# Optimization experiments

Measured on AMD Instinct MI355X. Metric: run time of the kernel, lower is better.

Reference implementation:

```python
import jax, jax.numpy as jnp
import numpy as np

KP_VARIANCE = 0.01


def make_coordinate_grid(h, w, dtype):
    # Normalized coordinates in [-1, 1], last dim is (x, y) as in monkey-net.
    x = 2.0 * (jnp.arange(w, dtype=dtype) / (w - 1)) - 1.0
    y = 2.0 * (jnp.arange(h, dtype=dtype) / (h - 1)) - 1.0
    xx = jnp.broadcast_to(x[None, :], (h, w))
    yy = jnp.broadcast_to(y[:, None], (h, w))
    return jnp.stack([xx, yy], axis=-1)  # (h, w, 2)


def grid_sample_bilinear(img, grid):
    # img: (N, C, H, W), grid: (N, Hg, Wg, 2) with xy in [-1, 1].
    # Bilinear, align_corners=True, zero padding (torch grid_sample defaults in monkey-net era).
    N, C, H, W = img.shape
    x = (grid[..., 0] + 1.0) * (W - 1) * 0.5
    y = (grid[..., 1] + 1.0) * (H - 1) * 0.5
    x0 = jnp.floor(x); y0 = jnp.floor(y)
    x1 = x0 + 1.0;     y1 = y0 + 1.0
    wx1 = x - x0; wx0 = 1.0 - wx1
    wy1 = y - y0; wy0 = 1.0 - wy1

    def gather(ix, iy):
        valid = ((ix >= 0) & (ix <= W - 1) & (iy >= 0) & (iy <= H - 1)).astype(img.dtype)
        ixc = jnp.clip(ix, 0, W - 1).astype(jnp.int32)
        iyc = jnp.clip(iy, 0, H - 1).astype(jnp.int32)
        vals = jax.vmap(lambda im, yy_, xx_: im[:, yy_, xx_])(img, iyc, ixc)  # (N, C, Hg, Wg)
        return vals * valid[:, None, :, :]

    out = (gather(x0, y0) * (wx0 * wy0)[:, None]
           + gather(x1, y0) * (wx1 * wy0)[:, None]
           + gather(x0, y1) * (wx0 * wy1)[:, None]
           + gather(x1, y1) * (wx1 * wy1)[:, None])
    return out


def setup_inputs() -> dict:
    key = jax.random.key(0)
    k1, k2, k3 = jax.random.split(key, 3)
    bs, c, dsrc, h, w = 4, 3, 1, 128, 128
    d, K = 8, 10
    source_image = jax.random.uniform(k1, (bs, c, dsrc, h, w), jnp.float32)
    kp_driving_mean = jax.random.uniform(k2, (bs, d, K, 2), jnp.float32, minval=-1.0, maxval=1.0)
    kp_source_mean = jax.random.uniform(k3, (bs, d, K, 2), jnp.float32, minval=-1.0, maxval=1.0)
    return {"source_image": source_image,
            "kp_driving_mean": kp_driving_mean,
            "kp_source_mean": kp_source_mean}


def reference(source_image, kp_driving_mean, kp_source_mean):
    bs, c, dsrc, h, w = source_image.shape
    _, d, K, _ = kp_driving_mean.shape
    grid = make_coordinate_grid(h, w, source_image.dtype)  # (h, w, 2)

    # Gaussian heatmaps around driving keypoints: (bs, d, K, h, w)
    diff2 = ((grid - kp_driving_mean[:, :, :, None, None, :]) ** 2).sum(-1)
    heat = jnp.exp(-0.5 * diff2 / KP_VARIANCE)
    heat = heat / heat.sum(axis=(-2, -1), keepdims=True)  # norm_const == 'sum'
    # add background feature map (zeros) as kp index 0
    heat = jnp.concatenate([jnp.zeros((bs, d, 1, h, w), heat.dtype), heat], axis=2)
    K1 = K + 1

    # keypoint motion difference: (bs, d, K1, 2)
    kp_diff = kp_source_mean - kp_driving_mean
    kp_diff = jnp.concatenate([jnp.zeros((bs, d, 1, 2), kp_diff.dtype), kp_diff], axis=2)
    diff_map = jnp.broadcast_to(kp_diff[:, :, :, :, None, None], (bs, d, K1, 2, h, w))

    # deformed source image per (frame, keypoint)
    app = jnp.broadcast_to(source_image[:, None, None], (bs, d, K1, c, dsrc, h, w))
    app = app.reshape(bs * d * K1, c * dsrc, h, w)
    deform = grid[None] + kp_diff.reshape(bs * d * K1, 1, 1, 2)  # (N, h, w, 2)
    deformed = grid_sample_bilinear(app, deform).reshape(bs, d, K1, c * dsrc, h, w)

    enc = jnp.concatenate([heat[:, :, :, None], diff_map, deformed], axis=3)  # (bs,d,K1,1+2+c,h,w)
    enc = enc.reshape(bs, d, -1, h, w)
    enc = jnp.transpose(enc, (0, 2, 1, 3, 4))  # (bs, out_channels, d, h, w)
    return enc
```

## Files before the change

### kernel.cpp

```cpp
#include <hip/hip_runtime.h>
#include <math.h>

#define BS 4
#define C  3
#define D  8
#define K  10
#define K1 11
#define H  128
#define W  128
#define HW (H*W)

typedef float float4a __attribute__((ext_vector_type(4), aligned(4)));

__global__ void memb_norm_kernel(const float* __restrict__ kpd,
                                 float* __restrict__ norm) {
    int idx = blockIdx.x;
    float kx = kpd[idx * 2 + 0];
    float ky = kpd[idx * 2 + 1];
    int lane = threadIdx.x;
    float sx = 0.f, sy = 0.f;
    #pragma unroll
    for (int j = lane; j < W; j += 64) {
        float coord = (float)j * (2.0f / 127.0f) - 1.0f;
        float ddx = coord - kx;
        float ddy = coord - ky;
        sx += __expf(-50.0f * ddx * ddx);
        sy += __expf(-50.0f * ddy * ddy);
    }
    #pragma unroll
    for (int o = 32; o > 0; o >>= 1) {
        sx += __shfl_down(sx, o, 64);
        sy += __shfl_down(sy, o, 64);
    }
    if (lane == 0) norm[idx] = 1.0f / (sx * sy);
}

__global__ void memb_main_kernel(const float* __restrict__ src,
                                 const float* __restrict__ kpd,
                                 const float* __restrict__ kps,
                                 const float* __restrict__ norm,
                                 float* __restrict__ out) {
    int rk = blockIdx.y;
    int k  = rk % K1;
    int r  = rk / K1;
    int di = r & (D - 1);
    int b  = r >> 3;

    float kx = 0.f, ky = 0.f, dx = 0.f, dy = 0.f, nrm = 0.f;
    if (k > 0) {
        int kidx = r * K + (k - 1);
        kx  = kpd[kidx * 2 + 0];
        ky  = kpd[kidx * 2 + 1];
        dx  = kps[kidx * 2 + 0] - kx;
        dy  = kps[kidx * 2 + 1] - ky;
        nrm = norm[kidx];
    }

    int p   = (blockIdx.x * blockDim.x + threadIdx.x) << 2;
    int wi0 = p & (W - 1);
    int hi  = p >> 7;

    float y  = (float)hi * (2.0f / 127.0f) - 1.0f;
    float ey = y - ky;
    float expy = __expf(-50.0f * ey * ey) * nrm;
    float heat[4];
    #pragma unroll
    for (int j = 0; j < 4; j++) {
        float x  = (float)(wi0 + j) * (2.0f / 127.0f) - 1.0f;
        float ex = x - kx;
        heat[j] = expy * __expf(-50.0f * ex * ex);
    }

    float cx = 63.5f * dx, cy = 63.5f * dy;
    float fsx = floorf(cx), fsy = floorf(cy);
    float fx = cx - fsx,    fy = cy - fsy;
    int   sx = (int)fsx,    sy = (int)fsy;
    float wx0 = 1.0f - fx,  wx1 = fx;

    int iy0 = hi + sy, iy1 = iy0 + 1;
    float rv0 = (iy0 >= 0 && iy0 < H) ? (1.0f - fy) : 0.0f;
    float rv1 = (iy1 >= 0 && iy1 < H) ? fy : 0.0f;
    int cy0 = min(max(iy0, 0), H - 1);
    int cy1 = min(max(iy1, 0), H - 1);

    int c0 = wi0 + sx;
    const float* sb = src + (size_t)b * C * HW;

    float v[C][4];
    if (c0 >= 0 && c0 <= W - 5) {
        #pragma unroll
        for (int ci = 0; ci < C; ci++) {
            const float* r0 = sb + ci * HW + cy0 * W;
            const float* r1 = sb + ci * HW + cy1 * W;
            float4a a  = *(const float4a*)(r0 + c0);
            float   a4 = r0[c0 + 4];
            float4a bq = *(const float4a*)(r1 + c0);
            float   b4 = r1[c0 + 4];
            float m0 = rv0 * a[0] + rv1 * bq[0];
            float m1 = rv0 * a[1] + rv1 * bq[1];
            float m2 = rv0 * a[2] + rv1 * bq[2];
            float m3 = rv0 * a[3] + rv1 * bq[3];
            float m4 = rv0 * a4   + rv1 * b4;
            v[ci][0] = wx0 * m0 + wx1 * m1;
            v[ci][1] = wx0 * m1 + wx1 * m2;
            v[ci][2] = wx0 * m2 + wx1 * m3;
            v[ci][3] = wx0 * m3 + wx1 * m4;
        }
    } else {
        #pragma unroll
        for (int ci = 0; ci < C; ci++) {
            const float* r0 = sb + ci * HW + cy0 * W;
            const float* r1 = sb + ci * HW + cy1 * W;
            float m[5];
            #pragma unroll
            for (int i = 0; i < 5; i++) {
                int q = c0 + i;
                bool ok = (q >= 0) && (q < W);
                int qc = min(max(q, 0), W - 1);
                float mm = rv0 * r0[qc] + rv1 * r1[qc];
                m[i] = ok ? mm : 0.0f;
            }
            v[ci][0] = wx0 * m[0] + wx1 * m[1];
            v[ci][1] = wx0 * m[1] + wx1 * m[2];
            v[ci][2] = wx0 * m[2] + wx1 * m[3];
            v[ci][3] = wx0 * m[3] + wx1 * m[4];
        }
    }

    const size_t cs = (size_t)D * HW;
    size_t base = ((size_t)(b * 66 + k * 6) * D + di) * HW + (size_t)hi * W + wi0;
    *(float4*)(out + base + 0 * cs) = make_float4(heat[0], heat[1], heat[2], heat[3]);
    *(float4*)(out + base + 1 * cs) = make_float4(dx, dx, dx, dx);
    *(float4*)(out + base + 2 * cs) = make_float4(dy, dy, dy, dy);
    *(float4*)(out + base + 3 * cs) = make_float4(v[0][0], v[0][1], v[0][2], v[0][3]);
    *(float4*)(out + base + 4 * cs) = make_float4(v[1][0], v[1][1], v[1][2], v[1][3]);
    *(float4*)(out + base + 5 * cs) = make_float4(v[2][0], v[2][1], v[2][2], v[2][3]);
}

extern "C" void kernel_launch(void* const* d_in, const int* in_sizes, int n_in,
                              void* d_out, int out_size, void* d_ws, size_t ws_size,
                              hipStream_t stream) {
    const float* src = (const float*)d_in[0];
    const float* kpd = (const float*)d_in[1];
    const float* kps = (const float*)d_in[2];
    float* out  = (float*)d_out;
    float* norm = (float*)d_ws;

    memb_norm_kernel<<<BS * D * K, 64, 0, stream>>>(kpd, norm);

    dim3 grid(HW / (256 * 4), BS * D * K1);
    memb_main_kernel<<<grid, 256, 0, stream>>>(src, kpd, kps, norm, out);
}
```

Baseline: 149.8 us.

## Fuse norm computation into main kernel with shared-memory exp tables

Removes the separate normalization kernel: each block computes the per-keypoint x/y Gaussian tables in shared memory, reduces them to the normalization constant, and builds heatmaps from the separable tables. Each thread now produces 8 pixels instead of 4, with a tile of 16 rows per block and an early zero path for fully out-of-bounds samples. This saves one launch and most exp evaluations, at the cost of two block barriers and redundant table computation in every block.

```diff
diff --git a/kernel.cpp b/kernel.cpp
--- a/kernel.cpp
+++ b/kernel.cpp
@@ -12,129 +12,145 @@
 
 typedef float float4a __attribute__((ext_vector_type(4), aligned(4)));
 
-__global__ void memb_norm_kernel(const float* __restrict__ kpd,
-                                 float* __restrict__ norm) {
-    int idx = blockIdx.x;
-    float kx = kpd[idx * 2 + 0];
-    float ky = kpd[idx * 2 + 1];
-    int lane = threadIdx.x;
-    float sx = 0.f, sy = 0.f;
-    #pragma unroll
-    for (int j = lane; j < W; j += 64) {
-        float coord = (float)j * (2.0f / 127.0f) - 1.0f;
-        float ddx = coord - kx;
-        float ddy = coord - ky;
-        sx += __expf(-50.0f * ddx * ddx);
-        sy += __expf(-50.0f * ddy * ddy);
-    }
-    #pragma unroll
-    for (int o = 32; o > 0; o >>= 1) {
-        sx += __shfl_down(sx, o, 64);
-        sy += __shfl_down(sy, o, 64);
-    }
-    if (lane == 0) norm[idx] = 1.0f / (sx * sy);
-}
+__global__ __launch_bounds__(256) void memb_fused_kernel(
+        const float* __restrict__ src,
+        const float* __restrict__ kpd,
+        const float* __restrict__ kps,
+        float* __restrict__ out) {
+    __shared__ __align__(16) float s_expx[128];
+    __shared__ __align__(16) float s_expy[128];
+    __shared__ float s_red[4];
+    __shared__ float s_nrm;
 
-__global__ void memb_main_kernel(const float* __restrict__ src,
-                                 const float* __restrict__ kpd,
-                                 const float* __restrict__ kps,
-                                 const float* __restrict__ norm,
-                                 float* __restrict__ out) {
     int rk = blockIdx.y;
     int k  = rk % K1;
     int r  = rk / K1;
     int di = r & (D - 1);
     int b  = r >> 3;
 
-    float kx = 0.f, ky = 0.f, dx = 0.f, dy = 0.f, nrm = 0.f;
+    float kx = 0.f, ky = 0.f, dx = 0.f, dy = 0.f;
     if (k > 0) {
         int kidx = r * K + (k - 1);
-        kx  = kpd[kidx * 2 + 0];
-        ky  = kpd[kidx * 2 + 1];
-        dx  = kps[kidx * 2 + 0] - kx;
-        dy  = kps[kidx * 2 + 1] - ky;
-        nrm = norm[kidx];
+        kx = kpd[kidx * 2 + 0];
+        ky = kpd[kidx * 2 + 1];
+        dx = kps[kidx * 2 + 0] - kx;
+        dy = kps[kidx * 2 + 1] - ky;
     }
 
-    int p   = (blockIdx.x * blockDim.x + threadIdx.x) << 2;
-    int wi0 = p & (W - 1);
-    int hi  = p >> 7;
+    int tid = threadIdx.x;
 
-    float y  = (float)hi * (2.0f / 127.0f) - 1.0f;
-    float ey = y - ky;
-    float expy = __expf(-50.0f * ey * ey) * nrm;
-    float heat[4];
-    #pragma unroll
-    for (int j = 0; j < 4; j++) {
-        float x  = (float)(wi0 + j) * (2.0f / 127.0f) - 1.0f;
-        float ex = x - kx;
-        heat[j] = expy * __expf(-50.0f * ex * ex);
+    {
+        int j = tid & 127;
+        float coord = (float)j * (2.0f / 127.0f) - 1.0f;
+        float dd = coord - ((tid < 128) ? kx : ky);
+        float e = __expf(-50.0f * dd * dd);
+        if (tid < 128) s_expx[j] = e;
+        else           s_expy[j] = e;
+        #pragma unroll
+        for (int o = 32; o > 0; o >>= 1) e += __shfl_down(e, o, 64);
+        if ((tid & 63) == 0) s_red[tid >> 6] = e;
     }
+    __syncthreads();
+    if (tid == 0) {
+        float sumx = s_red[0] + s_red[1];
+        float sumy = s_red[2] + s_red[3];
+        s_nrm = (k > 0) ? (1.0f / (sumx * sumy)) : 0.0f;
+    }
+    __syncthreads();
+
+    int g   = tid >> 4;
+    int rr  = tid & 15;
+    int wi0 = g << 3;
+    int hi  = (blockIdx.x << 4) + rr;
+
+    float hy = s_expy[hi] * s_nrm;
 
     float cx = 63.5f * dx, cy = 63.5f * dy;
     float fsx = floorf(cx), fsy = floorf(cy);
     float fx = cx - fsx,    fy = cy - fsy;
-    int   sx = (int)fsx,    sy = (int)fsy;
+    int   sxi = (int)fsx,   syi = (int)fsy;
     float wx0 = 1.0f - fx,  wx1 = fx;
 
-    int iy0 = hi + sy, iy1 = iy0 + 1;
+    int iy0 = hi + syi, iy1 = iy0 + 1;
     float rv0 = (iy0 >= 0 && iy0 < H) ? (1.0f - fy) : 0.0f;
     float rv1 = (iy1 >= 0 && iy1 < H) ? fy : 0.0f;
     int cy0 = min(max(iy0, 0), H - 1);
     int cy1 = min(max(iy1, 0), H - 1);
+    int c0  = wi0 + sxi;
 
-    int c0 = wi0 + sx;
     const float* sb = src + (size_t)b * C * HW;
 
-    float v[C][4];
-    if (c0 >= 0 && c0 <= W - 5) {
+    float v[C][8];
+    bool rowzero = (rv0 == 0.0f) && (rv1 == 0.0f);
+    bool colzero = (c0 > W - 1) || (c0 + 8 < 0);
+    if (rowzero || colzero) {
+        #pragma unroll
+        for (int ci = 0; ci < C; ci++)
+            #pragma unroll
+            for (int j = 0; j < 8; j++) v[ci][j] = 0.0f;
+    } else if (c0 >= 0 && c0 <= W - 9) {
         #pragma unroll
         for (int ci = 0; ci < C; ci++) {
-            const float* r0 = sb + ci * HW + cy0 * W;
-            const float* r1 = sb + ci * HW + cy1 * W;
-            float4a a  = *(const float4a*)(r0 + c0);
-            float   a4 = r0[c0 + 4];
-            float4a bq = *(const float4a*)(r1 + c0);
-            float   b4 = r1[c0 + 4];
-            float m0 = rv0 * a[0] + rv1 * bq[0];
-            float m1 = rv0 * a[1] + rv1 * bq[1];
-            float m2 = rv0 * a[2] + rv1 * bq[2];
-            float m3 = rv0 * a[3] + rv1 * bq[3];
-            float m4 = rv0 * a4   + rv1 * b4;
-            v[ci][0] = wx0 * m0 + wx1 * m1;
-            v[ci][1] = wx0 * m1 + wx1 * m2;
-            v[ci][2] = wx0 * m2 + wx1 * m3;
-            v[ci][3] = wx0 * m3 + wx1 * m4;
+            const float* r0 = sb + ci * HW + cy0 * W + c0;
+            const float* r1 = sb + ci * HW + cy1 * W + c0;
+            float4a a0 = *(const float4a*)(r0);
+            float4a a1 = *(const float4a*)(r0 + 4);
+            float   a2 = r0[8];
+            float4a b0 = *(const float4a*)(r1);
+            float4a b1 = *(const float4a*)(r1 + 4);
+            float   b2 = r1[8];
+            float m[9];
+            m[0] = rv0 * a0[0] + rv1 * b0[0];
+            m[1] = rv0 * a0[1] + rv1 * b0[1];
+            m[2] = rv0 * a0[2] + rv1 * b0[2];
+            m[3] = rv0 * a0[3] + rv1 * b0[3];
+            m[4] = rv0 * a1[0] + rv1 * b1[0];
+            m[5] = rv0 * a1[1] + rv1 * b1[1];
+            m[6] = rv0 * a1[2] + rv1 * b1[2];
+            m[7] = rv0 * a1[3] + rv1 * b1[3];
+            m[8] = rv0 * a2    + rv1 * b2;
+            #pragma unroll
+            for (int j = 0; j < 8; j++)
+                v[ci][j] = wx0 * m[j] + wx1 * m[j + 1];
         }
     } else {
         #pragma unroll
         for (int ci = 0; ci < C; ci++) {
             const float* r0 = sb + ci * HW + cy0 * W;
             const float* r1 = sb + ci * HW + cy1 * W;
-            float m[5];
+            float m[9];
             #pragma unroll
-            for (int i = 0; i < 5; i++) {
+            for (int i = 0; i < 9; i++) {
                 int q = c0 + i;
                 bool ok = (q >= 0) && (q < W);
                 int qc = min(max(q, 0), W - 1);
                 float mm = rv0 * r0[qc] + rv1 * r1[qc];
                 m[i] = ok ? mm : 0.0f;
             }
-            v[ci][0] = wx0 * m[0] + wx1 * m[1];
-            v[ci][1] = wx0 * m[1] + wx1 * m[2];
-            v[ci][2] = wx0 * m[2] + wx1 * m[3];
-            v[ci][3] = wx0 * m[3] + wx1 * m[4];
+            #pragma unroll
+            for (int j = 0; j < 8; j++)
+                v[ci][j] = wx0 * m[j] + wx1 * m[j + 1];
         }
     }
 
+    float4a ex0 = *(const float4a*)&s_expx[wi0];
+    float4a ex1 = *(const float4a*)&s_expx[wi0 + 4];
+
     const size_t cs = (size_t)D * HW;
     size_t base = ((size_t)(b * 66 + k * 6) * D + di) * HW + (size_t)hi * W + wi0;
-    *(float4*)(out + base + 0 * cs) = make_float4(heat[0], heat[1], heat[2], heat[3]);
-    *(float4*)(out + base + 1 * cs) = make_float4(dx, dx, dx, dx);
-    *(float4*)(out + base + 2 * cs) = make_float4(dy, dy, dy, dy);
-    *(float4*)(out + base + 3 * cs) = make_float4(v[0][0], v[0][1], v[0][2], v[0][3]);
-    *(float4*)(out + base + 4 * cs) = make_float4(v[1][0], v[1][1], v[1][2], v[1][3]);
-    *(float4*)(out + base + 5 * cs) = make_float4(v[2][0], v[2][1], v[2][2], v[2][3]);
+    float* o0 = out + base;
+    *(float4*)(o0 + 0)          = make_float4(hy*ex0[0], hy*ex0[1], hy*ex0[2], hy*ex0[3]);
+    *(float4*)(o0 + 4)          = make_float4(hy*ex1[0], hy*ex1[1], hy*ex1[2], hy*ex1[3]);
+    *(float4*)(o0 + cs)         = make_float4(dx, dx, dx, dx);
+    *(float4*)(o0 + cs + 4)     = make_float4(dx, dx, dx, dx);
+    *(float4*)(o0 + 2*cs)       = make_float4(dy, dy, dy, dy);
+    *(float4*)(o0 + 2*cs + 4)   = make_float4(dy, dy, dy, dy);
+    *(float4*)(o0 + 3*cs)       = make_float4(v[0][0], v[0][1], v[0][2], v[0][3]);
+    *(float4*)(o0 + 3*cs + 4)   = make_float4(v[0][4], v[0][5], v[0][6], v[0][7]);
+    *(float4*)(o0 + 4*cs)       = make_float4(v[1][0], v[1][1], v[1][2], v[1][3]);
+    *(float4*)(o0 + 4*cs + 4)   = make_float4(v[1][4], v[1][5], v[1][6], v[1][7]);
+    *(float4*)(o0 + 5*cs)       = make_float4(v[2][0], v[2][1], v[2][2], v[2][3]);
+    *(float4*)(o0 + 5*cs + 4)   = make_float4(v[2][4], v[2][5], v[2][6], v[2][7]);
 }
 
 extern "C" void kernel_launch(void* const* d_in, const int* in_sizes, int n_in,
@@ -144,10 +160,7 @@
     const float* kpd = (const float*)d_in[1];
     const float* kps = (const float*)d_in[2];
     float* out  = (float*)d_out;
-    float* norm = (float*)d_ws;
 
-    memb_norm_kernel<<<BS * D * K, 64, 0, stream>>>(kpd, norm);
-
-    dim3 grid(HW / (256 * 4), BS * D * K1);
-    memb_main_kernel<<<grid, 256, 0, stream>>>(src, kpd, kps, norm, out);
+    dim3 grid(H / 16, BS * D * K1);
+    memb_fused_kernel<<<grid, 256, 0, stream>>>(src, kpd, kps, out);
 }
```

Result: no change. 152.6 us (+1.9%).
